# Kernel optimization log

Hardware: AMD Instinct MI355X
Metric: run time of the kernel (lower is better)

## Reference

```python
import jax, jax.numpy as jnp
import numpy as np

B, T, D, H = 4, 2048, 1024, 16
HD = D // H  # 64


def setup_inputs() -> dict:
    key = jax.random.key(0)
    ks = jax.random.split(key, 5)
    return {
        "x": jax.random.normal(ks[0], (B, T, D), dtype=jnp.float32),
        "W_qkv": jax.random.normal(ks[1], (D, 3 * D), dtype=jnp.float32) * 0.02,
        "b_qkv": jax.random.normal(ks[2], (3 * D,), dtype=jnp.float32) * 0.02,
        "W_out": jax.random.normal(ks[3], (D, D), dtype=jnp.float32) * 0.02,
        "b_out": jax.random.normal(ks[4], (D,), dtype=jnp.float32) * 0.02,
        "mask": 1,
    }


def reference(x, W_qkv, b_qkv, W_out, b_out, mask):
    # fused QKV projection: (B,T,3D)
    qkv = x @ W_qkv + b_qkv
    # torch layout: view (B,T,H,3*hd) then chunk last dim into q,k,v
    qkv = qkv.reshape(B, T, H, 3, HD)
    q = qkv[..., 0, :].transpose(0, 2, 1, 3)  # (B,H,T,hd)
    k = qkv[..., 1, :].transpose(0, 2, 1, 3)
    v = qkv[..., 2, :].transpose(0, 2, 1, 3)
    scores = jnp.einsum('bhqd,bhkd->bhqk', q, k) / jnp.sqrt(jnp.float32(HD))
    if mask:
        causal = jnp.triu(jnp.ones((T, T), dtype=bool), k=1)
        scores = jnp.where(causal[None, None], jnp.float32(-jnp.inf), scores)
    attn = jax.nn.softmax(scores, axis=-1)
    out = jnp.einsum('bhqk,bhkd->bhqd', attn, v)  # (B,H,T,hd)
    out = out.transpose(0, 2, 1, 3).reshape(B, T, D)
    return out @ W_out + b_out
```

## Files before the change

### kernel.cpp

```cpp
#include <hip/hip_runtime.h>

typedef unsigned short u16;
typedef __bf16 bf16x8 __attribute__((ext_vector_type(8)));
typedef float f32x4 __attribute__((ext_vector_type(4)));
typedef float f32x16 __attribute__((ext_vector_type(16)));

#define DEV __device__ __forceinline__

constexpr int Bb = 4, Tt = 2048, Dd = 1024, Hh = 16, HDd = 64;
constexpr int MM = Bb * Tt;
constexpr float QSCALE = 0.125f * 1.4426950408889634f;

DEV u16 f2bf(float f) {
  unsigned u = __float_as_uint(f);
  u += 0x7fffu + ((u >> 16) & 1u);
  return (u16)(u >> 16);
}

DEV unsigned cvtpk(float a, float b) {
  unsigned r;
  asm("v_cvt_pk_bf16_f32 %0, %1, %2" : "=v"(r) : "v"(a), "v"(b));
  return r;
}

DEV void pswap(unsigned& a, unsigned& b) {
  asm("v_permlane32_swap_b32 %0, %1" : "+v"(a), "+v"(b));
}

DEV void gload_lds16(const u16* g, u16* l) {
  __builtin_amdgcn_global_load_lds(
      (const __attribute__((address_space(1))) void*)g,
      (__attribute__((address_space(3))) void*)l, 16, 0, 0);
}

__global__ __launch_bounds__(256) void cast_x_kernel(const float* __restrict__ in,
                                                     u16* __restrict__ out, int n8) {
  int i = blockIdx.x * 256 + threadIdx.x;
  if (i >= n8) return;
  const float4* p = (const float4*)in + (size_t)i * 2;
  float4 v0 = p[0], v1 = p[1];
  union { u16 u[8]; uint4 v; } t;
  t.u[0] = f2bf(v0.x); t.u[1] = f2bf(v0.y); t.u[2] = f2bf(v0.z); t.u[3] = f2bf(v0.w);
  t.u[4] = f2bf(v1.x); t.u[5] = f2bf(v1.y); t.u[6] = f2bf(v1.z); t.u[7] = f2bf(v1.w);
  ((uint4*)out)[i] = t.v;
}

__global__ __launch_bounds__(256) void wcast_t_kernel(const float* __restrict__ in,
                                                      u16* __restrict__ out, int K, int N) {
  __shared__ float tile[32][33];
  int n0 = blockIdx.x * 32, k0 = blockIdx.y * 32;
  int tx = threadIdx.x & 31, ty = threadIdx.x >> 5;
  #pragma unroll
  for (int yy = ty; yy < 32; yy += 8)
    tile[yy][tx] = in[(size_t)(k0 + yy) * N + n0 + tx];
  __syncthreads();
  #pragma unroll
  for (int yy = ty; yy < 32; yy += 8)
    out[(size_t)(n0 + yy) * K + k0 + tx] = f2bf(tile[tx][yy]);
}

DEV void stage_tile(const u16* __restrict__ src, int row0, int k0, int ld, u16* lds) {
  int t = threadIdx.x, w = t >> 6;
  #pragma unroll
  for (int j = 0; j < 2; ++j) {
    int e = (j * 256 + t) * 8;
    int r = e >> 5;
    int slot = (e >> 3) & 3;
    int c = (slot ^ ((r >> 1) & 3)) << 3;
    gload_lds16(src + (size_t)(row0 + r) * ld + k0 + c, lds + j * 2048 + w * 512);
  }
}

template <int EPI>
__global__ __launch_bounds__(256) void gemm_bt_kernel(
    const u16* __restrict__ A, const u16* __restrict__ Bt,
    const float* __restrict__ bias, float* __restrict__ Cf,
    u16* __restrict__ Qb, u16* __restrict__ Kb, u16* __restrict__ Vtb,
    int M, int N, int Kd) {
  __shared__ __align__(16) u16 SH[24576];
  int nx = N >> 7;
  int bid = blockIdx.y * nx + blockIdx.x;
  int nwg = (M >> 7) * nx;
  int swz = (bid & 7) * (nwg >> 3) + (bid >> 3);
  int m0 = (swz / nx) * 128, n0 = (swz % nx) * 128;

  int tid = threadIdx.x, l = tid & 63, w = tid >> 6;
  int lo = l & 15, g = l >> 4;
  int wm = (w >> 1) * 64, wn = (w & 1) * 64;
  f32x4 acc[4][4] = {};
  int nk = Kd >> 5;
  stage_tile(A, m0, 0, Kd, SH);
  stage_tile(Bt, n0, 0, Kd, SH + 12288);
  stage_tile(A, m0, 32, Kd, SH + 4096);
  stage_tile(Bt, n0, 32, Kd, SH + 12288 + 4096);
  asm volatile("s_waitcnt vmcnt(4)" ::: "memory");
  __builtin_amdgcn_s_barrier();
  for (int kt = 0; kt < nk; ++kt) {
    if (kt + 2 < nk) {
      int bi = (kt + 2) % 3;
      stage_tile(A, m0, (kt + 2) * 32, Kd, SH + bi * 4096);
      stage_tile(Bt, n0, (kt + 2) * 32, Kd, SH + 12288 + bi * 4096);
    }
    const u16* Ac = SH + (kt % 3) * 4096;
    const u16* Bc = SH + 12288 + (kt % 3) * 4096;
    bf16x8 a[4], b[4];
    #pragma unroll
    for (int i = 0; i < 4; ++i) {
      int row = wm + i * 16 + lo;
      a[i] = *(const bf16x8*)&Ac[row * 32 + ((g ^ ((row >> 1) & 3)) << 3)];
    }
    #pragma unroll
    for (int j = 0; j < 4; ++j) {
      int row = wn + j * 16 + lo;
      b[j] = *(const bf16x8*)&Bc[row * 32 + ((g ^ ((row >> 1) & 3)) << 3)];
    }
    #pragma unroll
    for (int i = 0; i < 4; ++i)
      #pragma unroll
      for (int j = 0; j < 4; ++j)
        acc[i][j] = __builtin_amdgcn_mfma_f32_16x16x32_bf16(a[i], b[j], acc[i][j], 0, 0, 0);
    if (kt + 2 < nk) {
      asm volatile("s_waitcnt vmcnt(4)" ::: "memory");
    } else {
      asm volatile("s_waitcnt vmcnt(0)" ::: "memory");
    }
    __builtin_amdgcn_s_barrier();
  }
  if (EPI == 0) {
    u16* ep = SH + w * 4096;
    int nblk = n0 + wn;
    int hh = nblk / 192, which = (nblk % 192) >> 6;
    int mblk = m0 + wm;
    int b_ = mblk >> 11, t0 = mblk & (Tt - 1);
    if (which == 2) {
      #pragma unroll
      for (int j = 0; j < 4; ++j) {
        float bv = bias[nblk + j * 16 + lo];
        int rowp = j * 16 + lo;
        #pragma unroll
        for (int i = 0; i < 4; ++i) {
          int slotp = i * 2 + (g >> 1);
          #pragma unroll
          for (int r = 0; r < 4; ++r) {
            ep[rowp * 64 + ((slotp ^ (rowp & 7)) << 3) + (g & 1) * 4 + r] =
                f2bf(acc[i][j][r] + bv);
          }
        }
      }
      asm volatile("s_waitcnt lgkmcnt(0)" ::: "memory");
      u16* dst = Vtb + (size_t)(b_ * Hh + hh) * HDd * Tt + t0;
      #pragma unroll
      for (int s = 0; s < 8; ++s) {
        int row = s * 8 + (l >> 3);
        int phys = ((l & 7) ^ (row & 7)) << 3;
        uint4 v = *(const uint4*)&ep[row * 64 + phys];
        *(uint4*)(dst + (size_t)row * Tt + (l & 7) * 8) = v;
      }
    } else {
      float qs = (which == 0) ? QSCALE : 1.0f;
      #pragma unroll
      for (int j = 0; j < 4; ++j) {
        float bv = bias[nblk + j * 16 + lo];
        int slot = j * 2 + (lo >> 3);
        #pragma unroll
        for (int i = 0; i < 4; ++i) {
          #pragma unroll
          for (int r = 0; r < 4; ++r) {
            int lrow = i * 16 + g * 4 + r;
            ep[lrow * 64 + ((slot ^ (lrow & 7)) << 3) + (lo & 7)] =
                f2bf((acc[i][j][r] + bv) * qs);
          }
        }
      }
      asm volatile("s_waitcnt lgkmcnt(0)" ::: "memory");
      u16* dst = (which == 0) ? Qb : Kb;
      dst += ((size_t)(b_ * Hh + hh) * Tt + t0) * HDd;
      #pragma unroll
      for (int s = 0; s < 8; ++s) {
        int row = s * 8 + (l >> 3);
        int phys = ((l & 7) ^ (row & 7)) << 3;
        uint4 v = *(const uint4*)&ep[row * 64 + phys];
        *(uint4*)(dst + row * 64 + (l & 7) * 8) = v;
      }
    }
  } else {
    #pragma unroll
    for (int j = 0; j < 4; ++j) {
      int n = n0 + wn + j * 16 + lo;
      float bv = bias[n];
      #pragma unroll
      for (int i = 0; i < 4; ++i) {
        #pragma unroll
        for (int r = 0; r < 4; ++r) {
          int m = m0 + wm + i * 16 + g * 4 + r;
          Cf[(size_t)m * N + n] = acc[i][j][r] + bv;
        }
      }
    }
  }
}

DEV void stage64x64(const u16* __restrict__ g, size_t rstride, u16* lds) {
  int t = threadIdx.x, w = t >> 6;
  #pragma unroll
  for (int j = 0; j < 2; ++j) {
    int e = j * 256 + t;
    int r = e >> 3, p = e & 7;
    int lg = p ^ (r & 7);
    gload_lds16(g + (size_t)r * rstride + lg * 8, lds + (size_t)(j * 256 + w * 64) * 8);
  }
}

DEV void build_pfrags(const f32x16& s, bf16x8& f0, bf16x8& f1) {
  unsigned w0 = cvtpk(s[0], s[1]),  w1 = cvtpk(s[2], s[3]);
  unsigned w2 = cvtpk(s[4], s[5]),  w3 = cvtpk(s[6], s[7]);
  unsigned w4 = cvtpk(s[8], s[9]),  w5 = cvtpk(s[10], s[11]);
  unsigned w6 = cvtpk(s[12], s[13]), w7 = cvtpk(s[14], s[15]);
  pswap(w0, w2);
  pswap(w1, w3);
  pswap(w4, w6);
  pswap(w5, w7);
  union { unsigned u[4]; bf16x8 v; } t0, t1;
  t0.u[0] = w0; t0.u[1] = w1; t0.u[2] = w2; t0.u[3] = w3;
  t1.u[0] = w4; t1.u[1] = w5; t1.u[2] = w6; t1.u[3] = w7;
  f0 = t0.v; f1 = t1.v;
}

DEV void write_o(u16* __restrict__ O, size_t rowbase, const f32x16& o0,
                 const f32x16& o1, float L, int hf) {
  float inv = 1.0f / L;
  #pragma unroll
  for (int m = 0; m < 4; ++m) {
    uint2 v0, v1;
    v0.x = cvtpk(o0[4 * m] * inv,     o0[4 * m + 1] * inv);
    v0.y = cvtpk(o0[4 * m + 2] * inv, o0[4 * m + 3] * inv);
    *(uint2*)(O + rowbase + m * 8 + hf * 4) = v0;
    v1.x = cvtpk(o1[4 * m] * inv,     o1[4 * m + 1] * inv);
    v1.y = cvtpk(o1[4 * m + 2] * inv, o1[4 * m + 3] * inv);
    *(uint2*)(O + rowbase + 32 + m * 8 + hf * 4) = v1;
  }
}

__global__ __launch_bounds__(256) void attn_kernel(const u16* __restrict__ Q,
                                                   const u16* __restrict__ K,
                                                   const u16* __restrict__ Vt,
                                                   u16* __restrict__ O) {
  __shared__ __align__(16) u16 Ks[3][4096];
  __shared__ __align__(16) u16 Vs[3][4096];
  int p = blockIdx.y & 7;
  int bh = ((int)blockIdx.y >> 3) * 8 + (int)blockIdx.x;
  int b_ = bh >> 4, h = bh & 15;
  const u16* Qp = Q + (size_t)bh * Tt * HDd;
  const u16* Kp = K + (size_t)bh * Tt * HDd;
  const u16* Vp = Vt + (size_t)bh * HDd * Tt;
  int tid = threadIdx.x, w = tid >> 6, l = tid & 63;
  int lq = l & 31, hf = l >> 5;
  int JA = 15 - p, JB = p;
  int ntA = 2 * JA + 2, ntB = 2 * JB + 2, ntT = ntA + ntB;

  int q0 = 128 * JA + 32 * w;
  int qrow = q0 + lq;

  bf16x8 aq[4];
  #pragma unroll
  for (int s = 0; s < 4; ++s)
    aq[s] = *(const bf16x8*)(Qp + (size_t)qrow * HDd + s * 16 + hf * 8);

  f32x16 o0 = {}, o1 = {};
  float M = -1e30f, L = 0.f;

  stage64x64(Kp, HDd, Ks[0]);
  stage64x64(Vp, Tt, Vs[0]);
  stage64x64(Kp + (size_t)64 * HDd, HDd, Ks[1]);
  stage64x64(Vp + 64, Tt, Vs[1]);
  asm volatile("s_waitcnt vmcnt(4)" ::: "memory");
  __builtin_amdgcn_s_barrier();

  for (int it = 0; it < ntT; ++it) {
    if (it == ntA) {
      size_t rbA = ((size_t)b_ * Tt + qrow) * Dd + h * HDd;
      write_o(O, rbA, o0, o1, L, hf);
      #pragma unroll
      for (int r = 0; r < 16; ++r) { o0[r] = 0.f; o1[r] = 0.f; }
      M = -1e30f; L = 0.f;
      q0 = 128 * JB + 32 * w;
      qrow = q0 + lq;
      #pragma unroll
      for (int s = 0; s < 4; ++s)
        aq[s] = *(const bf16x8*)(Qp + (size_t)qrow * HDd + s * 16 + hf * 8);
    }
    if (it + 2 < ntT) {
      int t2 = it + 2;
      int nkt = (t2 < ntA ? t2 : t2 - ntA) * 64;
      int bi = t2 % 3;
      stage64x64(Kp + (size_t)nkt * HDd, HDd, Ks[bi]);
      stage64x64(Vp + nkt, Tt, Vs[bi]);
    }
    int kt = (it < ntA ? it : it - ntA) * 64;
    const u16* Kc = Ks[it % 3];
    const u16* Vc = Vs[it % 3];
    if (kt < q0 + 32) {
      f32x16 s0 = {}, s1 = {};
      int swz = lq & 7;
      __builtin_amdgcn_s_setprio(1);
      #pragma unroll
      for (int ds = 0; ds < 4; ++ds) {
        int slot = 2 * ds + hf;
        bf16x8 k0 = *(const bf16x8*)&Kc[lq * 64 + ((slot ^ swz) << 3)];
        bf16x8 k1 = *(const bf16x8*)&Kc[(32 + lq) * 64 + ((slot ^ swz) << 3)];
        s0 = __builtin_amdgcn_mfma_f32_32x32x16_bf16(k0, aq[ds], s0, 0, 0, 0);
        s1 = __builtin_amdgcn_mfma_f32_32x32x16_bf16(k1, aq[ds], s1, 0, 0, 0);
      }
      __builtin_amdgcn_s_setprio(0);
      if (kt + 63 > q0) {
        #pragma unroll
        for (int r = 0; r < 16; ++r) {
          int kg = kt + (r & 3) + 8 * (r >> 2) + 4 * hf;
          if (kg > qrow)      s0[r] = -INFINITY;
          if (kg + 32 > qrow) s1[r] = -INFINITY;
        }
      }
      float mx_[16];
      #pragma unroll
      for (int r = 0; r < 16; ++r) mx_[r] = fmaxf(s0[r], s1[r]);
      #pragma unroll
      for (int st = 8; st >= 1; st >>= 1)
        #pragma unroll
        for (int r = 0; r < 16; ++r) if (r < st) mx_[r] = fmaxf(mx_[r], mx_[r + st]);
      float mx = fmaxf(mx_[0], __shfl_xor(mx_[0], 32));
      float sc = 1.f;
      if (!__all(mx <= M + 8.f)) {
        float Mn = fmaxf(M, mx);
        sc = __builtin_amdgcn_exp2f(M - Mn);
        M = Mn;
        #pragma unroll
        for (int r = 0; r < 16; ++r) { o0[r] *= sc; o1[r] *= sc; }
      }
      #pragma unroll
      for (int r = 0; r < 16; ++r) {
        s0[r] = __builtin_amdgcn_exp2f(s0[r] - M);
        s1[r] = __builtin_amdgcn_exp2f(s1[r] - M);
      }
      float ls_[16];
      #pragma unroll
      for (int r = 0; r < 16; ++r) ls_[r] = s0[r] + s1[r];
      #pragma unroll
      for (int st = 8; st >= 1; st >>= 1)
        #pragma unroll
        for (int r = 0; r < 16; ++r) if (r < st) ls_[r] += ls_[r + st];
      float ls = ls_[0] + __shfl_xor(ls_[0], 32);
      L = L * sc + ls;
      bf16x8 pf0, pf1, pf2, pf3;
      build_pfrags(s0, pf0, pf1);
      build_pfrags(s1, pf2, pf3);
      __builtin_amdgcn_s_setprio(1);
      #pragma unroll
      for (int ks = 0; ks < 4; ++ks) {
        int slot = 2 * ks + hf;
        bf16x8 v0 = *(const bf16x8*)&Vc[lq * 64 + ((slot ^ swz) << 3)];
        bf16x8 v1 = *(const bf16x8*)&Vc[(32 + lq) * 64 + ((slot ^ swz) << 3)];
        bf16x8 pf = (ks == 0) ? pf0 : (ks == 1) ? pf1 : (ks == 2) ? pf2 : pf3;
        o0 = __builtin_amdgcn_mfma_f32_32x32x16_bf16(v0, pf, o0, 0, 0, 0);
        o1 = __builtin_amdgcn_mfma_f32_32x32x16_bf16(v1, pf, o1, 0, 0, 0);
      }
      __builtin_amdgcn_s_setprio(0);
    }
    if (it + 2 < ntT) {
      asm volatile("s_waitcnt vmcnt(4)" ::: "memory");
    } else {
      asm volatile("s_waitcnt vmcnt(0)" ::: "memory");
    }
    __builtin_amdgcn_s_barrier();
  }

  size_t rbB = ((size_t)b_ * Tt + qrow) * Dd + h * HDd;
  write_o(O, rbB, o0, o1, L, hf);
}

extern "C" void kernel_launch(void* const* d_in, const int* in_sizes, int n_in,
                              void* d_out, int out_size, void* d_ws, size_t ws_size,
                              hipStream_t stream) {
  const float* x    = (const float*)d_in[0];
  const float* Wqkv = (const float*)d_in[1];
  const float* bqkv = (const float*)d_in[2];
  const float* Wout = (const float*)d_in[3];
  const float* bout = (const float*)d_in[4];
  float* out = (float*)d_out;
  char* ws = (char*)d_ws;

  u16* xb    = (u16*)(ws + 0);
  u16* Ob    = (u16*)(ws + 0);
  u16* Wqkvt = (u16*)(ws + 16777216);
  u16* Woutt = (u16*)(ws + 23068672);
  u16* Qb    = (u16*)(ws + 25165824);
  u16* Kb    = (u16*)(ws + 41943040);
  u16* Vtb   = (u16*)(ws + 58720256);

  cast_x_kernel<<<4096, 256, 0, stream>>>(x, xb, (MM * Dd) / 8);
  wcast_t_kernel<<<dim3(96, 32), 256, 0, stream>>>(Wqkv, Wqkvt, Dd, 3 * Dd);
  wcast_t_kernel<<<dim3(32, 32), 256, 0, stream>>>(Wout, Woutt, Dd, Dd);
  gemm_bt_kernel<0><<<dim3(24, 64), 256, 0, stream>>>(
      xb, Wqkvt, bqkv, nullptr, Qb, Kb, Vtb, MM, 3 * Dd, Dd);
  attn_kernel<<<dim3(8, 64), 256, 0, stream>>>(Qb, Kb, Vtb, Ob);
  gemm_bt_kernel<1><<<dim3(8, 64), 256, 0, stream>>>(
      Ob, Woutt, bout, out, nullptr, nullptr, nullptr, MM, Dd, Dd);
}
```

Before: 180.1 us.

## Split attention KV tiles across two wave groups with LDS split-softmax merge

```diff
diff --git a/kernel.cpp b/kernel.cpp
--- a/kernel.cpp
+++ b/kernel.cpp
@@ -200,15 +200,11 @@
   }
 }
 
-DEV void stage64x64(const u16* __restrict__ g, size_t rstride, u16* lds) {
-  int t = threadIdx.x, w = t >> 6;
-  #pragma unroll
-  for (int j = 0; j < 2; ++j) {
-    int e = j * 256 + t;
-    int r = e >> 3, p = e & 7;
-    int lg = p ^ (r & 7);
-    gload_lds16(g + (size_t)r * rstride + lg * 8, lds + (size_t)(j * 256 + w * 64) * 8);
-  }
+DEV void stage512(const u16* __restrict__ g, size_t rstride, u16* lds) {
+  int t = threadIdx.x;
+  int r = t >> 3, pp = t & 7;
+  int lg = pp ^ (r & 7);
+  gload_lds16(g + (size_t)r * rstride + lg * 8, lds + (size_t)(t & ~63) * 8);
 }
 
 DEV void build_pfrags(const f32x16& s, bf16x8& f0, bf16x8& f1) {
@@ -241,12 +237,14 @@
   }
 }
 
-__global__ __launch_bounds__(256) void attn_kernel(const u16* __restrict__ Q,
+__global__ __launch_bounds__(512) void attn_kernel(const u16* __restrict__ Q,
                                                    const u16* __restrict__ K,
                                                    const u16* __restrict__ Vt,
                                                    u16* __restrict__ O) {
-  __shared__ __align__(16) u16 Ks[3][4096];
-  __shared__ __align__(16) u16 Vs[3][4096];
+  __shared__ __align__(16) u16 Ks[4][4096];
+  __shared__ __align__(16) u16 Vs[4][4096];
+  __shared__ float MLs[8][64][2];
+  __shared__ float OSs[4][64][8];
   int p = blockIdx.y & 7;
   int bh = ((int)blockIdx.y >> 3) * 8 + (int)blockIdx.x;
   int b_ = bh >> 4, h = bh & 15;
@@ -254,12 +252,15 @@
   const u16* Kp = K + (size_t)bh * Tt * HDd;
   const u16* Vp = Vt + (size_t)bh * HDd * Tt;
   int tid = threadIdx.x, w = tid >> 6, l = tid & 63;
+  int wq = w & 3, grp = w >> 2;
   int lq = l & 31, hf = l >> 5;
   int JA = 15 - p, JB = p;
-  int ntA = 2 * JA + 2, ntB = 2 * JB + 2, ntT = ntA + ntB;
-
-  int q0 = 128 * JA + 32 * w;
+  int ntA = 2 * JA + 2;
+  constexpr int ntT = 34;
+
+  int q0 = 128 * JA + 32 * wq;
   int qrow = q0 + lq;
+  int swz = lq & 7;
 
   bf16x8 aq[4];
   #pragma unroll
@@ -269,39 +270,74 @@
   f32x16 o0 = {}, o1 = {};
   float M = -1e30f, L = 0.f;
 
-  stage64x64(Kp, HDd, Ks[0]);
-  stage64x64(Vp, Tt, Vs[0]);
-  stage64x64(Kp + (size_t)64 * HDd, HDd, Ks[1]);
-  stage64x64(Vp + 64, Tt, Vs[1]);
-  asm volatile("s_waitcnt vmcnt(4)" ::: "memory");
+  stage512(Kp, HDd, Ks[0]);
+  stage512(Vp, Tt, Vs[0]);
+  stage512(Kp + (size_t)64 * HDd, HDd, Ks[1]);
+  stage512(Vp + 64, Tt, Vs[1]);
+  asm volatile("s_waitcnt vmcnt(0)" ::: "memory");
   __builtin_amdgcn_s_barrier();
 
-  for (int it = 0; it < ntT; ++it) {
-    if (it == ntA) {
-      size_t rbA = ((size_t)b_ * Tt + qrow) * Dd + h * HDd;
-      write_o(O, rbA, o0, o1, L, hf);
+  int jB = ntA >> 1;
+  for (int j = 0; j < ntT / 2; ++j) {
+    int t2 = 2 * j + 2;
+    if (t2 < ntT) {
+      int kt2 = (t2 < ntA ? t2 : t2 - ntA) * 64;
+      stage512(Kp + (size_t)kt2 * HDd, HDd, Ks[t2 & 3]);
+      stage512(Vp + kt2, Tt, Vs[t2 & 3]);
+      int t3 = t2 + 1;
+      int kt3 = (t3 < ntA ? t3 : t3 - ntA) * 64;
+      stage512(Kp + (size_t)kt3 * HDd, HDd, Ks[t3 & 3]);
+      stage512(Vp + kt3, Tt, Vs[t3 & 3]);
+    }
+    if (j == jB) {
+      MLs[w][l][0] = M; MLs[w][l][1] = L;
+      asm volatile("s_waitcnt lgkmcnt(0)" ::: "memory");
+      __builtin_amdgcn_s_barrier();
+      float Mb = MLs[w ^ 4][l][0], Lb = MLs[w ^ 4][l][1];
+      float Mstar = fmaxf(M, Mb);
+      float ss = __builtin_amdgcn_exp2f(M - Mstar);
+      float sb = __builtin_amdgcn_exp2f(Mb - Mstar);
+      float Lm = L * ss + Lb * sb;
+      #pragma unroll
+      for (int r = 0; r < 16; ++r) { o0[r] *= ss; o1[r] *= ss; }
+      #pragma unroll
+      for (int c = 0; c < 4; ++c) {
+        if (w >= 4) {
+          #pragma unroll
+          for (int k = 0; k < 8; ++k)
+            OSs[wq][l][k] = (c < 2) ? o0[(c & 1) * 8 + k] : o1[(c & 1) * 8 + k];
+        }
+        asm volatile("s_waitcnt lgkmcnt(0)" ::: "memory");
+        __builtin_amdgcn_s_barrier();
+        if (w < 4) {
+          #pragma unroll
+          for (int k = 0; k < 8; ++k) {
+            float v = OSs[wq][l][k];
+            if (c < 2) o0[(c & 1) * 8 + k] += v; else o1[(c & 1) * 8 + k] += v;
+          }
+        }
+        asm volatile("s_waitcnt lgkmcnt(0)" ::: "memory");
+        __builtin_amdgcn_s_barrier();
+      }
+      if (w < 4) {
+        size_t rbA = ((size_t)b_ * Tt + qrow) * Dd + h * HDd;
+        write_o(O, rbA, o0, o1, Lm, hf);
+      }
       #pragma unroll
       for (int r = 0; r < 16; ++r) { o0[r] = 0.f; o1[r] = 0.f; }
       M = -1e30f; L = 0.f;
-      q0 = 128 * JB + 32 * w;
+      q0 = 128 * JB + 32 * wq;
       qrow = q0 + lq;
       #pragma unroll
       for (int s = 0; s < 4; ++s)
         aq[s] = *(const bf16x8*)(Qp + (size_t)qrow * HDd + s * 16 + hf * 8);
     }
-    if (it + 2 < ntT) {
-      int t2 = it + 2;
-      int nkt = (t2 < ntA ? t2 : t2 - ntA) * 64;
-      int bi = t2 % 3;
-      stage64x64(Kp + (size_t)nkt * HDd, HDd, Ks[bi]);
-      stage64x64(Vp + nkt, Tt, Vs[bi]);
-    }
-    int kt = (it < ntA ? it : it - ntA) * 64;
-    const u16* Kc = Ks[it % 3];
-    const u16* Vc = Vs[it % 3];
+    int myt = 2 * j + grp;
+    int kt = (myt < ntA ? myt : myt - ntA) * 64;
+    const u16* Kc = Ks[myt & 3];
+    const u16* Vc = Vs[myt & 3];
     if (kt < q0 + 32) {
       f32x16 s0 = {}, s1 = {};
-      int swz = lq & 7;
       __builtin_amdgcn_s_setprio(1);
       #pragma unroll
       for (int ds = 0; ds < 4; ++ds) {
@@ -365,16 +401,43 @@
       }
       __builtin_amdgcn_s_setprio(0);
     }
-    if (it + 2 < ntT) {
-      asm volatile("s_waitcnt vmcnt(4)" ::: "memory");
-    } else {
-      asm volatile("s_waitcnt vmcnt(0)" ::: "memory");
-    }
+    asm volatile("s_waitcnt vmcnt(0)" ::: "memory");
     __builtin_amdgcn_s_barrier();
   }
 
-  size_t rbB = ((size_t)b_ * Tt + qrow) * Dd + h * HDd;
-  write_o(O, rbB, o0, o1, L, hf);
+  MLs[w][l][0] = M; MLs[w][l][1] = L;
+  asm volatile("s_waitcnt lgkmcnt(0)" ::: "memory");
+  __builtin_amdgcn_s_barrier();
+  float Mb = MLs[w ^ 4][l][0], Lb = MLs[w ^ 4][l][1];
+  float Mstar = fmaxf(M, Mb);
+  float ss = __builtin_amdgcn_exp2f(M - Mstar);
+  float sb = __builtin_amdgcn_exp2f(Mb - Mstar);
+  float Lm = L * ss + Lb * sb;
+  #pragma unroll
+  for (int r = 0; r < 16; ++r) { o0[r] *= ss; o1[r] *= ss; }
+  #pragma unroll
+  for (int c = 0; c < 4; ++c) {
+    if (w >= 4) {
+      #pragma unroll
+      for (int k = 0; k < 8; ++k)
+        OSs[wq][l][k] = (c < 2) ? o0[(c & 1) * 8 + k] : o1[(c & 1) * 8 + k];
+    }
+    asm volatile("s_waitcnt lgkmcnt(0)" ::: "memory");
+    __builtin_amdgcn_s_barrier();
+    if (w < 4) {
+      #pragma unroll
+      for (int k = 0; k < 8; ++k) {
+        float v = OSs[wq][l][k];
+        if (c < 2) o0[(c & 1) * 8 + k] += v; else o1[(c & 1) * 8 + k] += v;
+      }
+    }
+    asm volatile("s_waitcnt lgkmcnt(0)" ::: "memory");
+    __builtin_amdgcn_s_barrier();
+  }
+  if (w < 4) {
+    size_t rbB = ((size_t)b_ * Tt + qrow) * Dd + h * HDd;
+    write_o(O, rbB, o0, o1, Lm, hf);
+  }
 }
 
 extern "C" void kernel_launch(void* const* d_in, const int* in_sizes, int n_in,
@@ -401,7 +464,7 @@
   wcast_t_kernel<<<dim3(32, 32), 256, 0, stream>>>(Wout, Woutt, Dd, Dd);
   gemm_bt_kernel<0><<<dim3(24, 64), 256, 0, stream>>>(
       xb, Wqkvt, bqkv, nullptr, Qb, Kb, Vtb, MM, 3 * Dd, Dd);
-  attn_kernel<<<dim3(8, 64), 256, 0, stream>>>(Qb, Kb, Vtb, Ob);
+  attn_kernel<<<dim3(8, 64), 512, 0, stream>>>(Qb, Kb, Vtb, Ob);
   gemm_bt_kernel<1><<<dim3(8, 64), 256, 0, stream>>>(
       Ob, Woutt, bout, out, nullptr, nullptr, nullptr, MM, Dd, Dd);
 }
```

After: 179.4 us. Within noise of the previous version (-0.4%).
